# Kernel optimization log

Hardware: AMD Instinct MI355X
Metric: run time of the kernel (lower is better)

## Reference

```python
import jax, jax.numpy as jnp
import numpy as np

B, N, D_MODEL, H = 8, 1024, 768, 12
HD = D_MODEL // H  # head dim = 64
SCALE = D_MODEL ** (-0.5)  # NOTE: original scales by input_dim**-0.5, not head_dim**-0.5


def setup_inputs() -> dict:
    key = jax.random.key(0)
    k1, k2 = jax.random.split(key)
    x = jax.random.normal(k1, (B, N, D_MODEL), dtype=jnp.float32)
    # torch Linear weight is [out,in]; we store transposed [in,out] for x @ W
    w_qkv = jax.random.normal(k2, (D_MODEL, 3 * D_MODEL), dtype=jnp.float32) * (D_MODEL ** -0.5)
    b_qkv = jnp.zeros((3 * D_MODEL,), dtype=jnp.float32)
    return {"x": x, "w_qkv": w_qkv, "b_qkv": b_qkv}


def reference(x, w_qkv, b_qkv):
    # QKV projection: [B, N, 3*D]
    y = jnp.einsum("bnd,de->bne", x, w_qkv) + b_qkv
    # Faithful to einops 'b n (h d qkv) -> qkv b h n d': qkv is fastest-varying
    y = y.reshape(B, N, H, HD, 3)
    q = jnp.transpose(y[..., 0], (0, 2, 1, 3))  # [B, H, N, HD]
    k = jnp.transpose(y[..., 1], (0, 2, 1, 3))
    v = jnp.transpose(y[..., 2], (0, 2, 1, 3))
    energy = jnp.einsum("bhqd,bhkd->bhqk", q, k)
    attn = jax.nn.softmax(energy * SCALE, axis=-1)  # dropout is identity at eval
    out = jnp.einsum("bhqk,bhkd->bhqd", attn, v)
    # 'b h n d -> b n (h d)'
    return jnp.transpose(out, (0, 2, 1, 3)).reshape(B, N, D_MODEL)
```

## Files before the change

### kernel.cpp

```cpp
#include <hip/hip_runtime.h>
#include <hip/hip_bf16.h>
#include <stdint.h>

#define NB 8
#define NS 1024
#define DM 768
#define NH 12
#define DH 64
#define NE 2304
#define MTOT (NB*NS)

typedef unsigned short u16;
typedef __attribute__((ext_vector_type(8))) __bf16 bf16x8;
typedef __attribute__((ext_vector_type(4))) float floatx4;
typedef __attribute__((ext_vector_type(4))) uint32_t uint32x4;

#define WS_XB  0ull
#define WS_WT  12582912ull
#define WS_BR  16121856ull
#define WS_QB  16131072ull
#define WS_KB  28713984ull
#define WS_VT  41296896ull

#define QSC 0.05206490030275093f

__device__ __forceinline__ u16 f2bf(float f) {
  union { float f; uint32_t u; } v; v.f = f;
  uint32_t r = (v.u + 0x7fffu + ((v.u >> 16) & 1u)) >> 16;
  return (u16)r;
}

__device__ __forceinline__ void gload16(const void* g, void* l) {
  __builtin_amdgcn_global_load_lds(
      (const __attribute__((address_space(1))) void*)g,
      (__attribute__((address_space(3))) void*)l, 16, 0, 0);
}

__global__ void conv_x_kernel(const float4* __restrict__ x, u16* __restrict__ xb, int n4) {
  int i = blockIdx.x * blockDim.x + threadIdx.x;
  int stride = gridDim.x * blockDim.x;
  for (; i < n4; i += stride) {
    float4 v = x[i];
    ushort4 r;
    r.x = f2bf(v.x); r.y = f2bf(v.y); r.z = f2bf(v.z); r.w = f2bf(v.w);
    ((ushort4*)xb)[i] = r;
  }
}

__global__ void prep_bias_kernel(const float* __restrict__ b, float* __restrict__ br) {
  const int o = blockIdx.x * 256 + threadIdx.x;
  if (o < 3 * DM) {
    const int c = o / DM, n = o % DM;
    const int h = n >> 6, d = n & 63;
    float v = b[h * 192 + d * 3 + c];
    if (c == 0) v *= QSC;
    br[o] = v;
  }
}

__global__ void transpose_w_kernel(const float* __restrict__ w, u16* __restrict__ wt) {
  __shared__ float tile[32][33];
  const int e0 = blockIdx.x * 32, k0 = blockIdx.y * 32;
  const int tx = threadIdx.x, ty = threadIdx.y;
#pragma unroll
  for (int i = 0; i < 4; i++)
    tile[ty + i*8][tx] = w[(size_t)(k0 + ty + i*8) * NE + e0 + tx];
  __syncthreads();
#pragma unroll
  for (int i = 0; i < 4; i++) {
    const int e = e0 + ty + i*8;
    const int c = e % 3, h = e / 192, d = (e % 192) / 3;
    const float sc = (c == 0) ? QSC : 1.0f;
    wt[((size_t)c * DM + h*64 + d) * DM + k0 + tx] = f2bf(tile[tx][ty + i*8] * sc);
  }
}

__global__ __launch_bounds__(64, 4) void qkv_gemm_kernel(
    const u16* __restrict__ xb, const u16* __restrict__ wt,
    const float* __restrict__ br,
    u16* __restrict__ qb, u16* __restrict__ kb, u16* __restrict__ vtb) {
  __shared__ __align__(16) u16 a_lds[2][64 * 32];
  __shared__ __align__(16) u16 b_lds[2][64 * 32];
  const int t  = threadIdx.x;
  const int lq = t & 15, lg = t >> 4;

  const int bid    = (int)blockIdx.x;
  const int xcd    = bid & 7;
  const int within = bid >> 3;
  const int mi     = within & 15;
  const int ni     = within >> 4;
  const int m0     = (xcd * 16 + mi) * 64;
  const int cls    = ni / 12;
  const int nb     = ni % 12;
  const int n0     = nb * 64;

  floatx4 z = {0.f, 0.f, 0.f, 0.f};
  floatx4 acc[4][4];
#pragma unroll
  for (int i = 0; i < 4; i++)
#pragma unroll
    for (int j = 0; j < 4; j++) acc[i][j] = z;

  const int srow = t >> 2;
  const int scb  = (t & 3) ^ ((t >> 3) & 3);
  const u16* ga = xb + (size_t)m0 * DM + scb * 8;
  const u16* gb = wt + ((size_t)cls * DM + n0) * DM + scb * 8;
  const int rswz = (lq >> 1) & 3;

#define STAGE(buf, k0)                                                            \
  {                                                                               \
    _Pragma("unroll")                                                             \
    for (int i = 0; i < 4; i++) {                                                 \
      gload16(ga + (size_t)(i*16 + srow) * DM + (k0), (char*)a_lds[buf] + i*1024); \
      gload16(gb + (size_t)(i*16 + srow) * DM + (k0), (char*)b_lds[buf] + i*1024); \
    }                                                                             \
  }

#define COMPUTE(buf)                                                              \
  {                                                                               \
    bf16x8 af[4], bfr[4];                                                         \
    _Pragma("unroll")                                                             \
    for (int i = 0; i < 4; i++)                                                   \
      af[i] = *(const bf16x8*)((const char*)a_lds[buf] + (i*16 + lq)*64 + ((lg ^ rswz) * 16)); \
    _Pragma("unroll")                                                             \
    for (int j = 0; j < 4; j++)                                                   \
      bfr[j] = *(const bf16x8*)((const char*)b_lds[buf] + (j*16 + lq)*64 + ((lg ^ rswz) * 16)); \
    if (cls == 2) {                                                               \
      _Pragma("unroll")                                                           \
      for (int i = 0; i < 4; i++)                                                 \
        _Pragma("unroll")                                                         \
        for (int j = 0; j < 4; j++)                                               \
          acc[i][j] = __builtin_amdgcn_mfma_f32_16x16x32_bf16(bfr[j], af[i], acc[i][j], 0, 0, 0); \
    } else {                                                                      \
      _Pragma("unroll")                                                           \
      for (int i = 0; i < 4; i++)                                                 \
        _Pragma("unroll")                                                         \
        for (int j = 0; j < 4; j++)                                               \
          acc[i][j] = __builtin_amdgcn_mfma_f32_16x16x32_bf16(af[i], bfr[j], acc[i][j], 0, 0, 0); \
    }                                                                             \
  }

  STAGE(0, 0);
  int cur = 0;
  for (int kt = 0; kt < 23; ++kt) {
    asm volatile("s_waitcnt lgkmcnt(0)" ::: "memory");
    STAGE(cur ^ 1, 32 * (kt + 1));
    asm volatile("s_waitcnt vmcnt(8)" ::: "memory");
    COMPUTE(cur);
    cur ^= 1;
  }
  asm volatile("s_waitcnt vmcnt(0)" ::: "memory");
  COMPUTE(cur);
#undef STAGE
#undef COMPUTE

  if (cls != 2) {
    u16* dst = (cls == 0) ? qb : kb;
#pragma unroll
    for (int j = 0; j < 4; j++) {
      const int d  = j*16 + lq;
      const float bv = br[cls * DM + n0 + d];
#pragma unroll
      for (int i = 0; i < 4; i++) {
        const int mb = m0 + i*16 + lg*4;
#pragma unroll
        for (int r = 0; r < 4; r++) {
          const int m = mb + r;
          const int bb = m >> 10, nn = m & 1023;
          dst[(((size_t)(bb * NH + nb)) * NS + nn) * DH + d] = f2bf(acc[i][j][r] + bv);
        }
      }
    }
  } else {
#pragma unroll
    for (int j = 0; j < 4; j++) {
      float bvv[4];
#pragma unroll
      for (int r = 0; r < 4; r++)
        bvv[r] = br[2 * DM + n0 + j*16 + lg*4 + r];
#pragma unroll
      for (int i = 0; i < 4; i++) {
        const int m = m0 + i*16 + lq;
        const int bb = m >> 10, nn = m & 1023;
#pragma unroll
        for (int r = 0; r < 4; r++) {
          const int d = j*16 + lg*4 + r;
          vtb[(((size_t)(bb * NH + nb)) * DH + d) * NS + nn] = f2bf(acc[i][j][r] + bvv[r]);
        }
      }
    }
  }
}

__global__ __launch_bounds__(256) void attn_kernel(
    const u16* __restrict__ qb, const u16* __restrict__ kb,
    const u16* __restrict__ vtb, float* __restrict__ out) {
  __shared__ __align__(16) u16 k_lds[64 * 64];
  __shared__ __align__(16) u16 v_lds[64 * 64];

  const int t = threadIdx.x, w = t >> 6, l = t & 63;
  const int bh = blockIdx.x >> 3, qblk = blockIdx.x & 7;
  const int bb = bh / NH, h = bh % NH;
  const int q0 = qblk * 128 + w * 32;
  const int lq = l & 15, lg = l >> 4;

  bf16x8 qf[2][2];
#pragma unroll
  for (int qt = 0; qt < 2; qt++) {
    const u16* qrow = qb + ((size_t)bh * NS + q0 + qt*16 + lq) * DH;
#pragma unroll
    for (int ds = 0; ds < 2; ds++)
      qf[qt][ds] = *(const bf16x8*)&qrow[lg*8 + ds*32];
  }

  float m2[2]    = {4.0f, 4.0f};
  float lsumP[2] = {0.f, 0.f};
  floatx4 z = {0.f, 0.f, 0.f, 0.f};
  floatx4 o[2][4];
#pragma unroll
  for (int qt = 0; qt < 2; qt++)
#pragma unroll
    for (int dt = 0; dt < 4; dt++) o[qt][dt] = z;

  const int srow = t >> 3;
  const int scb  = (t & 7) ^ (srow & 7);

  for (int kt0 = 0; kt0 < 16; kt0++) {
    const int k0 = kt0 * 64;
    __syncthreads();
#pragma unroll
    for (int i = 0; i < 2; i++) {
      const int row = i*32 + srow;
      gload16(kb  + ((size_t)bh * NS + k0 + row) * DH + scb*8, (char*)k_lds + i*4096 + w*1024);
      gload16(vtb + ((size_t)bh * DH + row) * NS + k0 + scb*8, (char*)v_lds + i*4096 + w*1024);
    }
    __syncthreads();

#pragma unroll
    for (int half = 0; half < 2; half++) {
      bf16x8 kf[2][2];
#pragma unroll
      for (int kt = 0; kt < 2; kt++) {
        const int krow = half*32 + ((lq >> 2) << 3) + kt*4 + (lq & 3);
#pragma unroll
        for (int ds = 0; ds < 2; ds++)
          kf[kt][ds] = *(const bf16x8*)((const char*)k_lds + krow*128 + ((ds*4 + lg) ^ (krow & 7))*16);
      }
      bf16x8 vf[4];
#pragma unroll
      for (int dt = 0; dt < 4; dt++) {
        const int vrow = dt*16 + lq;
        vf[dt] = *(const bf16x8*)((const char*)v_lds + vrow*128 + ((half*4 + lg) ^ (vrow & 7))*16);
      }

#pragma unroll
      for (int qt = 0; qt < 2; qt++) {
        floatx4 st0 = z, st1 = z;
        st0 = __builtin_amdgcn_mfma_f32_16x16x32_bf16(kf[0][0], qf[qt][0], st0, 0, 0, 0);
        st0 = __builtin_amdgcn_mfma_f32_16x16x32_bf16(kf[0][1], qf[qt][1], st0, 0, 0, 0);
        st1 = __builtin_amdgcn_mfma_f32_16x16x32_bf16(kf[1][0], qf[qt][0], st1, 0, 0, 0);
        st1 = __builtin_amdgcn_mfma_f32_16x16x32_bf16(kf[1][1], qf[qt][1], st1, 0, 0, 0);

        float p[8];
#pragma unroll
        for (int r = 0; r < 4; r++) { p[r] = st0[r]; p[4 + r] = st1[r]; }
        const float pmax = fmaxf(fmaxf(fmaxf(p[0], p[1]), fmaxf(p[2], p[3])),
                                 fmaxf(fmaxf(p[4], p[5]), fmaxf(p[6], p[7])));

        if (!__all(pmax - m2[qt] <= 8.0f)) {
          float mt = pmax;
          mt = fmaxf(mt, __shfl_xor(mt, 16));
          mt = fmaxf(mt, __shfl_xor(mt, 32));
          const float mnew = fmaxf(m2[qt], mt);
          const float corr = exp2f(m2[qt] - mnew);
          lsumP[qt] *= corr;
          float cr[4];
#pragma unroll
          for (int r = 0; r < 4; r++) cr[r] = __shfl(corr, lg*4 + r);
#pragma unroll
          for (int dt = 0; dt < 4; dt++)
#pragma unroll
            for (int r = 0; r < 4; r++) o[qt][dt][r] *= cr[r];
          m2[qt] = mnew;
        }

        const float m = m2[qt];
        float ls = 0.f;
        u16 pb[8];
#pragma unroll
        for (int e = 0; e < 8; e++) {
          const float pe = exp2f(p[e] - m);
          ls += pe;
          pb[e] = f2bf(pe);
        }
        lsumP[qt] += ls;

        uint32x4 pw;
        pw.x = (uint32_t)pb[0] | ((uint32_t)pb[1] << 16);
        pw.y = (uint32_t)pb[2] | ((uint32_t)pb[3] << 16);
        pw.z = (uint32_t)pb[4] | ((uint32_t)pb[5] << 16);
        pw.w = (uint32_t)pb[6] | ((uint32_t)pb[7] << 16);
        const bf16x8 pa = __builtin_bit_cast(bf16x8, pw);

#pragma unroll
        for (int dt = 0; dt < 4; dt++)
          o[qt][dt] = __builtin_amdgcn_mfma_f32_16x16x32_bf16(pa, vf[dt], o[qt][dt], 0, 0, 0);
      }
    }
  }

#pragma unroll
  for (int qt = 0; qt < 2; qt++) {
    float ls = lsumP[qt];
    ls += __shfl_xor(ls, 16);
    ls += __shfl_xor(ls, 32);
    const float inv = 1.0f / ls;
    float ir[4];
#pragma unroll
    for (int r = 0; r < 4; r++) ir[r] = __shfl(inv, lg*4 + r);
#pragma unroll
    for (int dt = 0; dt < 4; dt++)
#pragma unroll
      for (int r = 0; r < 4; r++) {
        const int n = q0 + qt*16 + lg*4 + r;
        out[((size_t)bb * NS + n) * DM + h*DH + dt*16 + lq] = o[qt][dt][r] * ir[r];
      }
  }
}

extern "C" void kernel_launch(void* const* d_in, const int* in_sizes, int n_in,
                              void* d_out, int out_size, void* d_ws, size_t ws_size,
                              hipStream_t stream) {
  const float* x     = (const float*)d_in[0];
  const float* w_qkv = (const float*)d_in[1];
  const float* b_qkv = (const float*)d_in[2];
  float* out = (float*)d_out;
  char* ws = (char*)d_ws;

  u16* xb   = (u16*)(ws + WS_XB);
  u16* wt   = (u16*)(ws + WS_WT);
  float* br = (float*)(ws + WS_BR);
  u16* qb   = (u16*)(ws + WS_QB);
  u16* kb   = (u16*)(ws + WS_KB);
  u16* vtb  = (u16*)(ws + WS_VT);

  conv_x_kernel<<<1024, 256, 0, stream>>>((const float4*)x, xb, MTOT * DM / 4);
  prep_bias_kernel<<<9, 256, 0, stream>>>(b_qkv, br);
  transpose_w_kernel<<<dim3(NE/32, DM/32), dim3(32, 8), 0, stream>>>(w_qkv, wt);
  qkv_gemm_kernel<<<4608, 64, 0, stream>>>(xb, wt, br, qb, kb, vtb);
  attn_kernel<<<(NB*NH) * (NS/128), 256, 0, stream>>>(qb, kb, vtb, out);
}
```

Before: 133.3 us.

## Double-buffer K/V tiles in LDS to overlap global loads with attention compute

The attention kernel now keeps two LDS buffers for K and V. It issues the async global-to-LDS loads for the next 64-key tile before computing on the current one, and synchronises with explicit waitcnt and barriers at the end of each iteration. This hides global load latency behind the MFMA and softmax work. In exchange LDS use doubles, which may lower occupancy, and each iteration now has two barriers.

```diff
diff --git a/kernel.cpp b/kernel.cpp
--- a/kernel.cpp
+++ b/kernel.cpp
@@ -195,8 +195,8 @@
 __global__ __launch_bounds__(256) void attn_kernel(
     const u16* __restrict__ qb, const u16* __restrict__ kb,
     const u16* __restrict__ vtb, float* __restrict__ out) {
-  __shared__ __align__(16) u16 k_lds[64 * 64];
-  __shared__ __align__(16) u16 v_lds[64 * 64];
+  __shared__ __align__(16) u16 k_lds[2][64 * 64];
+  __shared__ __align__(16) u16 v_lds[2][64 * 64];
 
   const int t = threadIdx.x, w = t >> 6, l = t & 63;
   const int bh = blockIdx.x >> 3, qblk = blockIdx.x & 7;
@@ -225,16 +225,28 @@
   const int srow = t >> 3;
   const int scb  = (t & 7) ^ (srow & 7);
 
+#define ASTAGE(buf, k0)                                                           \
+  {                                                                               \
+    _Pragma("unroll")                                                             \
+    for (int i = 0; i < 2; i++) {                                                 \
+      const int row = i*32 + srow;                                                \
+      gload16(kb  + ((size_t)bh * NS + (k0) + row) * DH + scb*8,                  \
+              (char*)k_lds[buf] + i*4096 + w*1024);                               \
+      gload16(vtb + ((size_t)bh * DH + row) * NS + (k0) + scb*8,                  \
+              (char*)v_lds[buf] + i*4096 + w*1024);                               \
+    }                                                                             \
+  }
+
+  ASTAGE(0, 0);
+  asm volatile("s_waitcnt vmcnt(0)" ::: "memory");
+  __builtin_amdgcn_s_barrier();
+
+  int cur = 0;
   for (int kt0 = 0; kt0 < 16; kt0++) {
-    const int k0 = kt0 * 64;
-    __syncthreads();
-#pragma unroll
-    for (int i = 0; i < 2; i++) {
-      const int row = i*32 + srow;
-      gload16(kb  + ((size_t)bh * NS + k0 + row) * DH + scb*8, (char*)k_lds + i*4096 + w*1024);
-      gload16(vtb + ((size_t)bh * DH + row) * NS + k0 + scb*8, (char*)v_lds + i*4096 + w*1024);
-    }
-    __syncthreads();
+    if (kt0 < 15) ASTAGE(cur ^ 1, (kt0 + 1) * 64);
+
+    const char* kl = (const char*)k_lds[cur];
+    const char* vl = (const char*)v_lds[cur];
 
 #pragma unroll
     for (int half = 0; half < 2; half++) {
@@ -244,13 +256,13 @@
         const int krow = half*32 + ((lq >> 2) << 3) + kt*4 + (lq & 3);
 #pragma unroll
         for (int ds = 0; ds < 2; ds++)
-          kf[kt][ds] = *(const bf16x8*)((const char*)k_lds + krow*128 + ((ds*4 + lg) ^ (krow & 7))*16);
+          kf[kt][ds] = *(const bf16x8*)(kl + krow*128 + ((ds*4 + lg) ^ (krow & 7))*16);
       }
       bf16x8 vf[4];
 #pragma unroll
       for (int dt = 0; dt < 4; dt++) {
         const int vrow = dt*16 + lq;
-        vf[dt] = *(const bf16x8*)((const char*)v_lds + vrow*128 + ((half*4 + lg) ^ (vrow & 7))*16);
+        vf[dt] = *(const bf16x8*)(vl + vrow*128 + ((half*4 + lg) ^ (vrow & 7))*16);
       }
 
 #pragma unroll
@@ -307,7 +319,14 @@
           o[qt][dt] = __builtin_amdgcn_mfma_f32_16x16x32_bf16(pa, vf[dt], o[qt][dt], 0, 0, 0);
       }
     }
-  }
+
+    asm volatile("s_waitcnt lgkmcnt(0)" ::: "memory");
+    __builtin_amdgcn_s_barrier();
+    if (kt0 < 15) asm volatile("s_waitcnt vmcnt(0)" ::: "memory");
+    __builtin_amdgcn_s_barrier();
+    cur ^= 1;
+  }
+#undef ASTAGE
 
 #pragma unroll
   for (int qt = 0; qt < 2; qt++) {
```

After: 136.0 us. No clear change (+2.0%).
